# Performance work log

Hardware: AMD Instinct MI355X
Metric: run time of the kernel (lower is better)

## Reference

```python
import math
import jax, jax.numpy as jnp
import numpy as np

N_HEADS = 16

def setup_inputs() -> dict:
    key = jax.random.key(0)
    k1, k2, k3 = jax.random.split(key, 3)
    B, S, D = 2, 2048, 1024
    x = jax.random.normal(k1, (B, S, D), dtype=jnp.float32)
    W_qkv = jax.random.normal(k2, (3 * D, D), dtype=jnp.float32)
    W_o = jax.random.normal(k3, (D, D), dtype=jnp.float32)
    return {"x": x, "W_qkv": W_qkv, "W_o": W_o}


def reference(x, W_qkv, W_o):
    B, S, D = x.shape
    H = N_HEADS
    d_h = D // H
    # fused QKV projection: (B,S,3D)
    t = jnp.matmul(x, W_qkv.T)
    t = t.reshape(B, S, 3, D)
    # NOTE: module reshapes (B,S,D) -> (B,H,S,d_h) directly (no transpose);
    # heads partition the flattened seq*feature layout. Replicate exactly.
    q = t[:, :, 0, :].reshape(B, H, S, d_h)
    k = t[:, :, 1, :].reshape(B, H, S, d_h)
    v = t[:, :, 2, :].reshape(B, H, S, d_h)
    # scaled by sqrt(d_model), as in the original (not sqrt(d_h))
    scores = jnp.einsum('bhqd,bhkd->bhqk', q, k) / math.sqrt(D)
    scores = jnp.tril(scores)
    # original sets ALL exact zeros to -inf (masks upper triangle)
    scores = jnp.where(scores == 0, -jnp.inf, scores)
    attn = jax.nn.softmax(scores, axis=-1)
    y_prime = jnp.matmul(attn, v)  # (B,H,S,d_h)
    y_prime = y_prime.transpose(0, 2, 1, 3).reshape(B, S, D)
    y = jnp.matmul(y_prime, W_o.T)
    return y
```

## Files before the change

kernel.cpp:

```cpp
#include <hip/hip_runtime.h>
#include <hip/hip_bf16.h>


using bf16 = __hip_bfloat16;
typedef __attribute__((ext_vector_type(8))) short bf16x8v;
typedef __attribute__((ext_vector_type(4))) float f32x4;

#define MFMA_BF16(A, B, C) __builtin_amdgcn_mfma_f32_16x16x32_bf16((A), (B), (C), 0, 0, 0)

#define GLD_LDS16(g, l)                                                        \
  __builtin_amdgcn_global_load_lds(                                            \
      (const __attribute__((address_space(1))) void*)(g),                      \
      (__attribute__((address_space(3))) void*)(l), 16, 0, 0)

static __device__ __forceinline__ unsigned short bf_bits(float f) {
  bf16 b = __float2bfloat16(f);
  return *reinterpret_cast<unsigned short*>(&b);
}

__global__ __launch_bounds__(256) void cvt_split(const float* __restrict__ in,
                                                 bf16* __restrict__ hi,
                                                 bf16* __restrict__ lo, int n) {
  int i = (blockIdx.x * 256 + threadIdx.x) * 4;
  if (i >= n) return;
  const float4 v = *(const float4*)(in + i);
  float vv[4] = {v.x, v.y, v.z, v.w};
  ushort4 hb, lb;
  unsigned short* hp = &hb.x;
  unsigned short* lp = &lb.x;
#pragma unroll
  for (int j = 0; j < 4; ++j) {
    bf16 h = __float2bfloat16(vv[j]);
    float r = vv[j] - __bfloat162float(h);
    hp[j] = bf_bits(vv[j]);
    lp[j] = bf_bits(r);
  }
  *(ushort4*)(hi + i) = hb;
  *(ushort4*)(lo + i) = lb;
}

__global__ __launch_bounds__(256) void cvt_plain(const float* __restrict__ in,
                                                 bf16* __restrict__ out, int n) {
  int i = (blockIdx.x * 256 + threadIdx.x) * 4;
  if (i >= n) return;
  const float4 v = *(const float4*)(in + i);
  ushort4 ob;
  ob.x = bf_bits(v.x); ob.y = bf_bits(v.y); ob.z = bf_bits(v.z); ob.w = bf_bits(v.w);
  *(ushort4*)(out + i) = ob;
}

__global__ __launch_bounds__(256) void gemm_qkv(
    const bf16* __restrict__ Ah, const bf16* __restrict__ Al,
    const bf16* __restrict__ Bh, const bf16* __restrict__ Bl,
    bf16* __restrict__ Qhi, bf16* __restrict__ Qlo,
    bf16* __restrict__ Khi, bf16* __restrict__ Klo,
    bf16* __restrict__ Vt) {
  const int K = 1024;
  const int NT = 24;
  __shared__ __attribute__((aligned(16))) bf16 AsH[4096], AsL[4096], BsH[4096], BsL[4096];
  const int t = threadIdx.x;
  const int lane = t & 63;
  const int wave = t >> 6;
  const int wr = wave >> 1, wc = wave & 1;
  int bid = blockIdx.x;
  bid = (bid & 7) * (768 >> 3) + (bid >> 3);
  const int bm = bid / NT, bn = bid % NT;
  const int brow = bm * 128, bcol = bn * 128;
  const bf16* pAh = Ah + (size_t)brow * K;
  const bf16* pAl = Al + (size_t)brow * K;
  const bf16* pBh = Bh + (size_t)bcol * K;
  const bf16* pBl = Bl + (size_t)bcol * K;
  const int r0 = t >> 2;
  const int c0 = (t & 3) * 8;
  f32x4 acc[4][4] = {};
  for (int k0 = 0; k0 < K; k0 += 32) {
    __syncthreads();
    GLD_LDS16(pAh + (size_t)r0 * K + k0 + c0,        &AsH[t * 8]);
    GLD_LDS16(pAh + (size_t)(r0 + 64) * K + k0 + c0, &AsH[2048 + t * 8]);
    GLD_LDS16(pAl + (size_t)r0 * K + k0 + c0,        &AsL[t * 8]);
    GLD_LDS16(pAl + (size_t)(r0 + 64) * K + k0 + c0, &AsL[2048 + t * 8]);
    GLD_LDS16(pBh + (size_t)r0 * K + k0 + c0,        &BsH[t * 8]);
    GLD_LDS16(pBh + (size_t)(r0 + 64) * K + k0 + c0, &BsH[2048 + t * 8]);
    GLD_LDS16(pBl + (size_t)r0 * K + k0 + c0,        &BsL[t * 8]);
    GLD_LDS16(pBl + (size_t)(r0 + 64) * K + k0 + c0, &BsL[2048 + t * 8]);
    __syncthreads();
    bf16x8v ah[4], al[4], bh_[4], bl_[4];
    const int ao = (wr * 64 + (lane & 15)) * 32 + (lane >> 4) * 8;
    const int bo = (wc * 64 + (lane & 15)) * 32 + (lane >> 4) * 8;
#pragma unroll
    for (int i = 0; i < 4; ++i) {
      ah[i]  = *(const bf16x8v*)&AsH[ao + i * 512];
      al[i]  = *(const bf16x8v*)&AsL[ao + i * 512];
      bh_[i] = *(const bf16x8v*)&BsH[bo + i * 512];
      bl_[i] = *(const bf16x8v*)&BsL[bo + i * 512];
    }
#pragma unroll
    for (int i = 0; i < 4; ++i)
#pragma unroll
      for (int j = 0; j < 4; ++j) {
        acc[i][j] = MFMA_BF16(ah[i], bh_[j], acc[i][j]);
        acc[i][j] = MFMA_BF16(ah[i], bl_[j], acc[i][j]);
        acc[i][j] = MFMA_BF16(al[i], bh_[j], acc[i][j]);
      }
  }
#pragma unroll
  for (int i = 0; i < 4; ++i)
#pragma unroll
    for (int j = 0; j < 4; ++j)
#pragma unroll
      for (int e = 0; e < 4; ++e) {
        const int m = brow + wr * 64 + i * 16 + ((lane >> 4) << 2) + e;
        const int n = bcol + wc * 64 + j * 16 + (lane & 15);
        float v = acc[i][j][e];
        const int b = m >> 11, s = m & 2047;
        const int c = n >> 10, d = n & 1023;
        const int bh_i = (b << 4) | (s >> 7);
        const int s2 = ((s & 127) << 4) | (d >> 6);
        const int dh = d & 63;
        if (c == 2) {
          Vt[((size_t)bh_i << 17) | ((size_t)dh << 11) | (size_t)s2] = __float2bfloat16(v);
        } else {
          if (c == 0) v *= 0.03125f;
          const size_t idx = ((size_t)bh_i << 17) | ((size_t)s2 << 6) | (size_t)dh;
          bf16 hv = __float2bfloat16(v);
          bf16 lv = __float2bfloat16(v - __bfloat162float(hv));
          if (c == 0) { Qhi[idx] = hv; Qlo[idx] = lv; }
          else        { Khi[idx] = hv; Klo[idx] = lv; }
        }
      }
}

__global__ __launch_bounds__(64) void attn_kernel(
    const bf16* __restrict__ Qhi, const bf16* __restrict__ Qlo,
    const bf16* __restrict__ Khi, const bf16* __restrict__ Klo,
    const bf16* __restrict__ Vt, bf16* __restrict__ Yp) {
  const int lane = threadIdx.x & 63;
  const int bh = blockIdx.x & 31;
  const int c  = 63 - (blockIdx.x >> 5);
  const int b = bh >> 4, h = bh & 15;
  const size_t base = (size_t)bh << 17;
  const bf16* qh_p = Qhi + base;
  const bf16* ql_p = Qlo + base;
  const bf16* kh_p = Khi + base;
  const bf16* kl_p = Klo + base;
  const bf16* v_p  = Vt + base;
  const int qbase = c << 5;
  const int l15 = lane & 15;
  const int lg  = lane >> 4;
  __shared__ __attribute__((aligned(16))) bf16 Plds[32][72];

  bf16x8v qfh[2][2], qfl[2][2];
#pragma unroll
  for (int q2 = 0; q2 < 2; ++q2)
#pragma unroll
    for (int x2 = 0; x2 < 2; ++x2) {
      const size_t o = (size_t)(qbase + q2 * 16 + l15) * 64 + x2 * 32 + lg * 8;
      qfh[q2][x2] = *(const bf16x8v*)(qh_p + o);
      qfl[q2][x2] = *(const bf16x8v*)(ql_p + o);
    }
  bf16x8v ones8;
#pragma unroll
  for (int j = 0; j < 8; ++j) ones8[j] = (short)0x3F80;

  f32x4 oac[2][4] = {};
  f32x4 oden[2] = {};
  float mrun[2] = {-3.0e38f, -3.0e38f};
  const float L2E = 1.4426950408889634f;
  const int nfull = c >> 1;

  for (int kt = 0; kt <= nfull; ++kt) {
    const int kb = kt << 6;
    f32x4 st[4][2] = {};
#pragma unroll
    for (int kf = 0; kf < 4; ++kf) {
      const size_t ko = (size_t)(kb + kf * 16 + l15) * 64 + lg * 8;
      const bf16x8v kh0 = *(const bf16x8v*)(kh_p + ko);
      const bf16x8v kh1 = *(const bf16x8v*)(kh_p + ko + 32);
      const bf16x8v kl0 = *(const bf16x8v*)(kl_p + ko);
      const bf16x8v kl1 = *(const bf16x8v*)(kl_p + ko + 32);
#pragma unroll
      for (int q2 = 0; q2 < 2; ++q2) {
        f32x4 a = st[kf][q2];
        a = MFMA_BF16(kh0, qfh[q2][0], a);
        a = MFMA_BF16(kh1, qfh[q2][1], a);
        a = MFMA_BF16(kh0, qfl[q2][0], a);
        a = MFMA_BF16(kh1, qfl[q2][1], a);
        a = MFMA_BF16(kl0, qfh[q2][0], a);
        a = MFMA_BF16(kl1, qfh[q2][1], a);
        st[kf][q2] = a;
      }
    }
    if (kt == nfull) {
#pragma unroll
      for (int kf = 0; kf < 4; ++kf)
#pragma unroll
        for (int q2 = 0; q2 < 2; ++q2)
#pragma unroll
          for (int e = 0; e < 4; ++e) {
            const int key = kb + kf * 16 + (lg << 2) + e;
            const int qr  = qbase + q2 * 16 + l15;
            if (key > qr) st[kf][q2][e] = -3.0e38f;
          }
    }
    float tmax[2] = {-3.0e38f, -3.0e38f};
#pragma unroll
    for (int kf = 0; kf < 4; ++kf)
#pragma unroll
      for (int q2 = 0; q2 < 2; ++q2)
#pragma unroll
        for (int e = 0; e < 4; ++e)
          tmax[q2] = fmaxf(tmax[q2], st[kf][q2][e]);
#pragma unroll
    for (int q2 = 0; q2 < 2; ++q2) {
      tmax[q2] = fmaxf(tmax[q2], __shfl_xor(tmax[q2], 16));
      tmax[q2] = fmaxf(tmax[q2], __shfl_xor(tmax[q2], 32));
    }
    const int ok = (tmax[0] <= mrun[0] + 8.0f) && (tmax[1] <= mrun[1] + 8.0f);
    if (!__all(ok)) {
      float sfac[2];
#pragma unroll
      for (int q2 = 0; q2 < 2; ++q2) {
        const float mn = fmaxf(mrun[q2], tmax[q2]);
        sfac[q2] = exp2f((mrun[q2] - mn) * L2E);
        mrun[q2] = mn;
      }
#pragma unroll
      for (int q2 = 0; q2 < 2; ++q2)
#pragma unroll
        for (int e = 0; e < 4; ++e) {
          const float so = __shfl(sfac[q2], (lg << 2) + e);
          oden[q2][e] *= so;
#pragma unroll
          for (int df = 0; df < 4; ++df) oac[q2][df][e] *= so;
        }
    }
    const float mL0 = mrun[0] * L2E, mL1 = mrun[1] * L2E;
#pragma unroll
    for (int kf = 0; kf < 4; ++kf)
#pragma unroll
      for (int q2 = 0; q2 < 2; ++q2) {
        const float mL = q2 ? mL1 : mL0;
        ushort4 pk;
        unsigned short* pp = &pk.x;
#pragma unroll
        for (int e = 0; e < 4; ++e) {
          const float pv = exp2f(fmaf(st[kf][q2][e], L2E, -mL));
          pp[e] = bf_bits(pv);
        }
        *(ushort4*)&Plds[q2 * 16 + l15][kf * 16 + (lg << 2)] = pk;
      }
    __syncthreads();
#pragma unroll
    for (int x2 = 0; x2 < 2; ++x2) {
      bf16x8v pa[2];
#pragma unroll
      for (int q2 = 0; q2 < 2; ++q2)
        pa[q2] = *(const bf16x8v*)&Plds[q2 * 16 + l15][x2 * 32 + lg * 8];
#pragma unroll
      for (int q2 = 0; q2 < 2; ++q2)
        oden[q2] = MFMA_BF16(pa[q2], ones8, oden[q2]);
#pragma unroll
      for (int df = 0; df < 4; ++df) {
        const bf16x8v vb =
            *(const bf16x8v*)(v_p + (size_t)(df * 16 + l15) * 2048 + kb + x2 * 32 + lg * 8);
#pragma unroll
        for (int q2 = 0; q2 < 2; ++q2)
          oac[q2][df] = MFMA_BF16(pa[q2], vb, oac[q2][df]);
      }
    }
  }
#pragma unroll
  for (int q2 = 0; q2 < 2; ++q2) {
    float li[4];
#pragma unroll
    for (int e = 0; e < 4; ++e) li[e] = 1.0f / oden[q2][e];
#pragma unroll
    for (int df = 0; df < 4; ++df)
#pragma unroll
      for (int e = 0; e < 4; ++e) {
        const int qr = qbase + q2 * 16 + (lg << 2) + e;
        const int dh = df * 16 + l15;
        Yp[(size_t)(b * 2048 + qr) * 1024 + h * 64 + dh] =
            __float2bfloat16(oac[q2][df][e] * li[e]);
      }
  }
}

__global__ __launch_bounds__(256) void gemm_out(const bf16* __restrict__ A,
                                                const bf16* __restrict__ B,
                                                float* __restrict__ C) {
  const int K = 1024;
  const int NT = 8;
  __shared__ __attribute__((aligned(16))) bf16 As[4096], Bs[4096];
  const int t = threadIdx.x;
  const int lane = t & 63;
  const int wave = t >> 6;
  const int wr = wave >> 1, wc = wave & 1;
  int bid = blockIdx.x;
  bid = (bid & 7) * (256 >> 3) + (bid >> 3);
  const int bm = bid / NT, bn = bid % NT;
  const int brow = bm * 128, bcol = bn * 128;
  const bf16* pA = A + (size_t)brow * K;
  const bf16* pB = B + (size_t)bcol * K;
  const int r0 = t >> 2;
  const int c0 = (t & 3) * 8;
  f32x4 acc[4][4] = {};
  for (int k0 = 0; k0 < K; k0 += 32) {
    __syncthreads();
    GLD_LDS16(pA + (size_t)r0 * K + k0 + c0,        &As[t * 8]);
    GLD_LDS16(pA + (size_t)(r0 + 64) * K + k0 + c0, &As[2048 + t * 8]);
    GLD_LDS16(pB + (size_t)r0 * K + k0 + c0,        &Bs[t * 8]);
    GLD_LDS16(pB + (size_t)(r0 + 64) * K + k0 + c0, &Bs[2048 + t * 8]);
    __syncthreads();
    bf16x8v af[4], bf_[4];
    const int ao = (wr * 64 + (lane & 15)) * 32 + (lane >> 4) * 8;
    const int bo = (wc * 64 + (lane & 15)) * 32 + (lane >> 4) * 8;
#pragma unroll
    for (int i = 0; i < 4; ++i) {
      af[i]  = *(const bf16x8v*)&As[ao + i * 512];
      bf_[i] = *(const bf16x8v*)&Bs[bo + i * 512];
    }
#pragma unroll
    for (int i = 0; i < 4; ++i)
#pragma unroll
      for (int j = 0; j < 4; ++j)
        acc[i][j] = MFMA_BF16(af[i], bf_[j], acc[i][j]);
  }
#pragma unroll
  for (int i = 0; i < 4; ++i)
#pragma unroll
    for (int j = 0; j < 4; ++j)
#pragma unroll
      for (int e = 0; e < 4; ++e) {
        const int m = brow + wr * 64 + i * 16 + ((lane >> 4) << 2) + e;
        const int n = bcol + wc * 64 + j * 16 + (lane & 15);
        C[(size_t)m * 1024 + n] = acc[i][j][e];
      }
}

extern "C" void kernel_launch(void* const* d_in, const int* in_sizes, int n_in,
                              void* d_out, int out_size, void* d_ws, size_t ws_size,
                              hipStream_t stream) {
  (void)in_sizes; (void)n_in; (void)out_size; (void)ws_size;
  const float* x    = (const float*)d_in[0];
  const float* wqkv = (const float*)d_in[1];
  const float* wo   = (const float*)d_in[2];
  float* out = (float*)d_out;

  const size_t NX = 4096ull * 1024;
  const size_t NW = 3072ull * 1024;
  const size_t NO = 1024ull * 1024;

  bf16* p = (bf16*)d_ws;
  bf16* xh  = p; p += NX;
  bf16* xl  = p; p += NX;
  bf16* wqh = p; p += NW;
  bf16* wql = p; p += NW;
  bf16* wob = p; p += NO;
  bf16* qhi = p; p += NX;
  bf16* qlo = p; p += NX;
  bf16* khi = p; p += NX;
  bf16* klo = p; p += NX;
  bf16* vt  = p; p += NX;
  bf16* yp  = p; p += NX;

  hipLaunchKernelGGL(cvt_split, dim3(NX / 1024), dim3(256), 0, stream, x, xh, xl, (int)NX);
  hipLaunchKernelGGL(cvt_split, dim3(NW / 1024), dim3(256), 0, stream, wqkv, wqh, wql, (int)NW);
  hipLaunchKernelGGL(cvt_plain, dim3(NO / 1024), dim3(256), 0, stream, wo, wob, (int)NO);
  hipLaunchKernelGGL(gemm_qkv, dim3(32 * 24), dim3(256), 0, stream,
                     xh, xl, wqh, wql, qhi, qlo, khi, klo, vt);
  hipLaunchKernelGGL(attn_kernel, dim3(2048), dim3(64), 0, stream,
                     qhi, qlo, khi, klo, vt, yp);
  hipLaunchKernelGGL(gemm_out, dim3(32 * 8), dim3(256), 0, stream, yp, wob, out);
}
```

Measured before the change: 337.6 us.

## Skip split-precision terms for V projection and prefetch K/V tiles in attention

In the QKV GEMM, blocks producing V columns skip loading the low bf16 parts and run only the hi*hi MFMA, since V is stored as plain bf16 anyway. In the attention kernel, K fragments for the next tile are software-prefetched into registers and V fragments are loaded before the softmax. The single-wave __syncthreads is replaced by an lgkmcnt wait plus a sched barrier. Launch bounds request two blocks per SIMD. V loses the lo correction terms, which slightly reduces its accuracy, and the extra register buffers raise register pressure.

```diff
diff --git a/kernel.cpp b/kernel.cpp
--- a/kernel.cpp
+++ b/kernel.cpp
@@ -66,6 +66,7 @@
   bid = (bid & 7) * (768 >> 3) + (bid >> 3);
   const int bm = bid / NT, bn = bid % NT;
   const int brow = bm * 128, bcol = bn * 128;
+  const bool isV = (bcol >= 2048);
   const bf16* pAh = Ah + (size_t)brow * K;
   const bf16* pAl = Al + (size_t)brow * K;
   const bf16* pBh = Bh + (size_t)bcol * K;
@@ -77,31 +78,45 @@
     __syncthreads();
     GLD_LDS16(pAh + (size_t)r0 * K + k0 + c0,        &AsH[t * 8]);
     GLD_LDS16(pAh + (size_t)(r0 + 64) * K + k0 + c0, &AsH[2048 + t * 8]);
-    GLD_LDS16(pAl + (size_t)r0 * K + k0 + c0,        &AsL[t * 8]);
-    GLD_LDS16(pAl + (size_t)(r0 + 64) * K + k0 + c0, &AsL[2048 + t * 8]);
     GLD_LDS16(pBh + (size_t)r0 * K + k0 + c0,        &BsH[t * 8]);
     GLD_LDS16(pBh + (size_t)(r0 + 64) * K + k0 + c0, &BsH[2048 + t * 8]);
-    GLD_LDS16(pBl + (size_t)r0 * K + k0 + c0,        &BsL[t * 8]);
-    GLD_LDS16(pBl + (size_t)(r0 + 64) * K + k0 + c0, &BsL[2048 + t * 8]);
+    if (!isV) {
+      GLD_LDS16(pAl + (size_t)r0 * K + k0 + c0,        &AsL[t * 8]);
+      GLD_LDS16(pAl + (size_t)(r0 + 64) * K + k0 + c0, &AsL[2048 + t * 8]);
+      GLD_LDS16(pBl + (size_t)r0 * K + k0 + c0,        &BsL[t * 8]);
+      GLD_LDS16(pBl + (size_t)(r0 + 64) * K + k0 + c0, &BsL[2048 + t * 8]);
+    }
     __syncthreads();
-    bf16x8v ah[4], al[4], bh_[4], bl_[4];
     const int ao = (wr * 64 + (lane & 15)) * 32 + (lane >> 4) * 8;
     const int bo = (wc * 64 + (lane & 15)) * 32 + (lane >> 4) * 8;
+    bf16x8v ah[4], bh_[4];
 #pragma unroll
     for (int i = 0; i < 4; ++i) {
       ah[i]  = *(const bf16x8v*)&AsH[ao + i * 512];
-      al[i]  = *(const bf16x8v*)&AsL[ao + i * 512];
       bh_[i] = *(const bf16x8v*)&BsH[bo + i * 512];
-      bl_[i] = *(const bf16x8v*)&BsL[bo + i * 512];
-    }
-#pragma unroll
-    for (int i = 0; i < 4; ++i)
-#pragma unroll
-      for (int j = 0; j < 4; ++j) {
-        acc[i][j] = MFMA_BF16(ah[i], bh_[j], acc[i][j]);
-        acc[i][j] = MFMA_BF16(ah[i], bl_[j], acc[i][j]);
-        acc[i][j] = MFMA_BF16(al[i], bh_[j], acc[i][j]);
-      }
+    }
+    if (!isV) {
+      bf16x8v al[4], bl_[4];
+#pragma unroll
+      for (int i = 0; i < 4; ++i) {
+        al[i]  = *(const bf16x8v*)&AsL[ao + i * 512];
+        bl_[i] = *(const bf16x8v*)&BsL[bo + i * 512];
+      }
+#pragma unroll
+      for (int i = 0; i < 4; ++i)
+#pragma unroll
+        for (int j = 0; j < 4; ++j) {
+          acc[i][j] = MFMA_BF16(ah[i], bh_[j], acc[i][j]);
+          acc[i][j] = MFMA_BF16(ah[i], bl_[j], acc[i][j]);
+          acc[i][j] = MFMA_BF16(al[i], bh_[j], acc[i][j]);
+        }
+    } else {
+#pragma unroll
+      for (int i = 0; i < 4; ++i)
+#pragma unroll
+        for (int j = 0; j < 4; ++j)
+          acc[i][j] = MFMA_BF16(ah[i], bh_[j], acc[i][j]);
+    }
   }
 #pragma unroll
   for (int i = 0; i < 4; ++i)
@@ -130,7 +145,7 @@
       }
 }
 
-__global__ __launch_bounds__(64) void attn_kernel(
+__global__ __launch_bounds__(64, 2) void attn_kernel(
     const bf16* __restrict__ Qhi, const bf16* __restrict__ Qlo,
     const bf16* __restrict__ Khi, const bf16* __restrict__ Klo,
     const bf16* __restrict__ Vt, bf16* __restrict__ Yp) {
@@ -168,28 +183,45 @@
   const float L2E = 1.4426950408889634f;
   const int nfull = c >> 1;
 
+  bf16x8v kh0r[4], kh1r[4], kl0r[4], kl1r[4];
+#define LOADK(kb_)                                                             \
+  {                                                                            \
+    const int _kb = (kb_);                                                     \
+    _Pragma("unroll")                                                          \
+    for (int kf = 0; kf < 4; ++kf) {                                           \
+      const size_t ko = (size_t)(_kb + kf * 16 + l15) * 64 + lg * 8;           \
+      kh0r[kf] = *(const bf16x8v*)(kh_p + ko);                                 \
+      kh1r[kf] = *(const bf16x8v*)(kh_p + ko + 32);                            \
+      kl0r[kf] = *(const bf16x8v*)(kl_p + ko);                                 \
+      kl1r[kf] = *(const bf16x8v*)(kl_p + ko + 32);                            \
+    }                                                                          \
+  }
+  LOADK(0);
+
   for (int kt = 0; kt <= nfull; ++kt) {
     const int kb = kt << 6;
     f32x4 st[4][2] = {};
 #pragma unroll
-    for (int kf = 0; kf < 4; ++kf) {
-      const size_t ko = (size_t)(kb + kf * 16 + l15) * 64 + lg * 8;
-      const bf16x8v kh0 = *(const bf16x8v*)(kh_p + ko);
-      const bf16x8v kh1 = *(const bf16x8v*)(kh_p + ko + 32);
-      const bf16x8v kl0 = *(const bf16x8v*)(kl_p + ko);
-      const bf16x8v kl1 = *(const bf16x8v*)(kl_p + ko + 32);
+    for (int kf = 0; kf < 4; ++kf)
 #pragma unroll
       for (int q2 = 0; q2 < 2; ++q2) {
         f32x4 a = st[kf][q2];
-        a = MFMA_BF16(kh0, qfh[q2][0], a);
-        a = MFMA_BF16(kh1, qfh[q2][1], a);
-        a = MFMA_BF16(kh0, qfl[q2][0], a);
-        a = MFMA_BF16(kh1, qfl[q2][1], a);
-        a = MFMA_BF16(kl0, qfh[q2][0], a);
-        a = MFMA_BF16(kl1, qfh[q2][1], a);
+        a = MFMA_BF16(kh0r[kf], qfh[q2][0], a);
+        a = MFMA_BF16(kh1r[kf], qfh[q2][1], a);
+        a = MFMA_BF16(kh0r[kf], qfl[q2][0], a);
+        a = MFMA_BF16(kh1r[kf], qfl[q2][1], a);
+        a = MFMA_BF16(kl0r[kf], qfh[q2][0], a);
+        a = MFMA_BF16(kl1r[kf], qfh[q2][1], a);
         st[kf][q2] = a;
       }
-    }
+    bf16x8v vreg[2][4];
+#pragma unroll
+    for (int x2 = 0; x2 < 2; ++x2)
+#pragma unroll
+      for (int df = 0; df < 4; ++df)
+        vreg[x2][df] =
+            *(const bf16x8v*)(v_p + (size_t)(df * 16 + l15) * 2048 + kb + x2 * 32 + lg * 8);
+    if (kt < nfull) LOADK(kb + 64);
     if (kt == nfull) {
 #pragma unroll
       for (int kf = 0; kf < 4; ++kf)
@@ -249,26 +281,28 @@
         }
         *(ushort4*)&Plds[q2 * 16 + l15][kf * 16 + (lg << 2)] = pk;
       }
-    __syncthreads();
+    asm volatile("s_waitcnt lgkmcnt(0)" ::: "memory");
+    __builtin_amdgcn_sched_barrier(0);
+    bf16x8v pa[2][2];
+#pragma unroll
+    for (int x2 = 0; x2 < 2; ++x2)
+#pragma unroll
+      for (int q2 = 0; q2 < 2; ++q2)
+        pa[x2][q2] = *(const bf16x8v*)&Plds[q2 * 16 + l15][x2 * 32 + lg * 8];
+    asm volatile("" ::: "memory");
 #pragma unroll
     for (int x2 = 0; x2 < 2; ++x2) {
-      bf16x8v pa[2];
 #pragma unroll
       for (int q2 = 0; q2 < 2; ++q2)
-        pa[q2] = *(const bf16x8v*)&Plds[q2 * 16 + l15][x2 * 32 + lg * 8];
-#pragma unroll
-      for (int q2 = 0; q2 < 2; ++q2)
-        oden[q2] = MFMA_BF16(pa[q2], ones8, oden[q2]);
-#pragma unroll
-      for (int df = 0; df < 4; ++df) {
-        const bf16x8v vb =
-            *(const bf16x8v*)(v_p + (size_t)(df * 16 + l15) * 2048 + kb + x2 * 32 + lg * 8);
+        oden[q2] = MFMA_BF16(pa[x2][q2], ones8, oden[q2]);
+#pragma unroll
+      for (int df = 0; df < 4; ++df)
 #pragma unroll
         for (int q2 = 0; q2 < 2; ++q2)
-          oac[q2][df] = MFMA_BF16(pa[q2], vb, oac[q2][df]);
-      }
-    }
-  }
+          oac[q2][df] = MFMA_BF16(pa[x2][q2], vreg[x2][df], oac[q2][df]);
+    }
+  }
+#undef LOADK
 #pragma unroll
   for (int q2 = 0; q2 < 2; ++q2) {
     float li[4];
```

Measured after the change: 320.3 us. -5.1%, faster.
